# Optimization experiments

Measured on AMD Instinct MI355X. Metric: run time of the kernel, lower is better.

## Reference

```python
import jax, jax.numpy as jnp
import numpy as np

B, N, F_, H = 4, 2048, 1024, 16
DH = F_ // H
SCALE = F_ / 19.5  # module uses feats/19.5, not sqrt(head_dim)


def setup_inputs() -> dict:
    key = jax.random.key(0)
    ks = jax.random.split(key, 9)
    s = 1.0 / np.sqrt(F_)
    return {
        "x": jax.random.normal(ks[0], (B, N, F_), jnp.float32),
        "Wq": jax.random.normal(ks[1], (F_, F_), jnp.float32) * s,
        "bq": jax.random.normal(ks[2], (F_,), jnp.float32) * s,
        "Wk": jax.random.normal(ks[3], (F_, F_), jnp.float32) * s,
        "bk": jax.random.normal(ks[4], (F_,), jnp.float32) * s,
        "Wv": jax.random.normal(ks[5], (F_, F_), jnp.float32) * s,
        "bv": jax.random.normal(ks[6], (F_,), jnp.float32) * s,
        "Wo": jax.random.normal(ks[7], (F_, F_), jnp.float32) * s,
        "bo": jax.random.normal(ks[8], (F_,), jnp.float32) * s,
    }


def reference(x, Wq, bq, Wk, bk, Wv, bv, Wo, bo):
    b, n, f = x.shape
    # torch Linear: x @ W.T + b; then view(b,n,h,dh).transpose(1,2) -> bhnd
    def proj(W, bias):
        return (x @ W.T + bias).reshape(b, n, H, DH).transpose(0, 2, 1, 3)

    q = proj(Wq, bq)  # [b,h,n,dh]
    k = proj(Wk, bk)
    v = proj(Wv, bv)
    score = jax.nn.softmax(jnp.einsum("bhif,bhjf->bhij", q, k) / SCALE, axis=-1)
    attn = jnp.einsum("bhij,bhjf->bihf", score, v)  # [b,n,h,dh]
    o = attn.reshape(b, n, f) @ Wo.T + bo  # dropout p=0.0 -> identity
    return o
```

## Files before the change

kernel.cpp:

```cpp
#include <hip/hip_runtime.h>
#include <stdint.h>

typedef unsigned short u16;
typedef __bf16 bf16x8 __attribute__((ext_vector_type(8)));
typedef float f32x4 __attribute__((ext_vector_type(4)));

#define QSCALE (19.5f/1024.0f * 1.44269504088896340736f)

#define EXPB 16251.0f

__device__ __forceinline__ u16 f2bf(float f){
  uint32_t u = __float_as_uint(f);
  return (u16)((u + 0x7FFFu + ((u >> 16) & 1u)) >> 16);
}

__device__ __forceinline__ uint64_t cvt4(float4 f){
  union{ u16 u[4]; uint64_t v; } pk;
  pk.u[0]=f2bf(f.x); pk.u[1]=f2bf(f.y); pk.u[2]=f2bf(f.z); pk.u[3]=f2bf(f.w);
  return pk.v;
}

#define GLD_LDS16(g,l) __builtin_amdgcn_global_load_lds( \
    (const __attribute__((address_space(1))) void*)(g),  \
    (__attribute__((address_space(3))) void*)(l), 16, 0, 0)

__global__ __launch_bounds__(256) void k_prep(
    const float4* __restrict__ x,  const float4* __restrict__ Wq,
    const float4* __restrict__ Wk, const float4* __restrict__ Wv,
    const float4* __restrict__ Wo,
    const float4* __restrict__ bq, const float4* __restrict__ bk, const float4* __restrict__ bv,
    uint64_t* __restrict__ xb, uint64_t* __restrict__ wqkv, uint64_t* __restrict__ wob,
    float4* __restrict__ bqkv)
{
  const int NX = 2097152, NW = 262144;
  const int total = NX + 4*NW + 768;
  int i = blockIdx.x*256 + threadIdx.x;
  const int stride = gridDim.x*256;
  for (; i < total; i += stride){
    if (i < NX)             xb[i] = cvt4(x[i]);
    else if (i < NX+NW)     { int j = i-NX;      wqkv[j]      = cvt4(Wq[j]); }
    else if (i < NX+2*NW)   { int j = i-NX-NW;   wqkv[NW+j]   = cvt4(Wk[j]); }
    else if (i < NX+3*NW)   { int j = i-NX-2*NW; wqkv[2*NW+j] = cvt4(Wv[j]); }
    else if (i < NX+4*NW)   { int j = i-NX-3*NW; wob[j]       = cvt4(Wo[j]); }
    else {
      int j = i - NX - 4*NW;
      bqkv[j] = (j < 256) ? bq[j] : (j < 512 ? bk[j-256] : bv[j-512]);
    }
  }
}

template<int MODE>
__global__ __launch_bounds__(256) void gemm_bt(
    const u16* __restrict__ A, const u16* __restrict__ Bw,
    const float* __restrict__ bias, float* __restrict__ Cout,
    u16* __restrict__ q_ws, u16* __restrict__ k_ws, u16* __restrict__ v_ws)
{
  __shared__ u16 lds[3*8192];
  const int tid  = threadIdx.x;
  const int w    = tid >> 6, lane = tid & 63;
  const int wr   = w >> 1,  wc   = w & 1;
  const int g    = lane >> 4, c16 = lane & 15;
  const int nt   = blockIdx.x, mt = blockIdx.y;
  const size_t arow0 = (size_t)mt * 128, brow0 = (size_t)nt * 128;

  f32x4 acc[4][4] = {};

  const int srow  = w*16 + (lane >> 2);
  const int schk  = ((lane & 3) ^ ((lane >> 2) & 3)) * 8;
  const u16* gA = A  + (arow0 + srow)*1024 + schk;
  const u16* gB = Bw + (brow0 + srow)*1024 + schk;

  u16* ldsA0 = &lds[w*512];
  u16* ldsB0 = &lds[4096 + w*512];

  const int rswz = (g ^ (c16 & 3)) * 8;
  const int abase = (wr*64 + c16)*32 + rswz;
  const int bbase = 4096 + (wc*64 + c16)*32 + rswz;

#define GSTAGE(B2) do{ \
    GLD_LDS16(gA,          ldsA0 + (B2)*8192); \
    GLD_LDS16(gA + 65536,  ldsA0 + (B2)*8192 + 2048); \
    GLD_LDS16(gB,          ldsB0 + (B2)*8192); \
    GLD_LDS16(gB + 65536,  ldsB0 + (B2)*8192 + 2048); \
    gA += 32; gB += 32; \
  }while(0)

#define GBODY(B, STG, VMW) do{ \
    if (STG) GSTAGE(((B)+2)%3); \
    bf16x8 af[4], bfr[4]; \
    _Pragma("unroll") \
    for (int m = 0; m < 4; m++) \
      af[m]  = __builtin_bit_cast(bf16x8, *(const uint4*)(&lds[(B)*8192 + abase + m*512])); \
    _Pragma("unroll") \
    for (int n = 0; n < 4; n++) \
      bfr[n] = __builtin_bit_cast(bf16x8, *(const uint4*)(&lds[(B)*8192 + bbase + n*512])); \
    __builtin_amdgcn_s_setprio(1); \
    _Pragma("unroll") \
    for (int m = 0; m < 4; m++) \
      _Pragma("unroll") \
      for (int n = 0; n < 4; n++) \
        acc[m][n] = __builtin_amdgcn_mfma_f32_16x16x32_bf16(af[m], bfr[n], acc[m][n], 0, 0, 0); \
    __builtin_amdgcn_s_setprio(0); \
    if ((VMW) == 4){ asm volatile("s_waitcnt vmcnt(4)" ::: "memory"); __builtin_amdgcn_s_barrier(); } \
    else if ((VMW) == 0){ asm volatile("s_waitcnt vmcnt(0)" ::: "memory"); __builtin_amdgcn_s_barrier(); } \
  }while(0)

  GSTAGE(0); GSTAGE(1);
  asm volatile("s_waitcnt vmcnt(4)" ::: "memory");
  __builtin_amdgcn_s_barrier();

  #pragma unroll 1
  for (int rr = 0; rr < 10; rr++){
    GBODY(0, 1, 4);
    GBODY(1, 1, 4);
    GBODY(2, 1, 4);
  }
  GBODY(0, 0, 0);
  GBODY(1, 0, -1);

#undef GBODY
#undef GSTAGE

  #pragma unroll
  for (int m = 0; m < 4; m++){
    const size_t i0 = arow0 + wr*64 + m*16 + g*4;
    #pragma unroll
    for (int n = 0; n < 4; n++){
      const int o = (int)brow0 + wc*64 + n*16 + c16;
      const float bias_v = bias[o];
      if (MODE == 0){
        const int proj = o >> 10, wi = o & 1023, hh = wi >> 6, dd = wi & 63;
        if (proj < 2){
          u16* base = (proj == 0) ? q_ws : k_ws;
          const float sc = (proj == 0) ? QSCALE : 1.0f;
          #pragma unroll
          for (int r = 0; r < 4; r++){
            const size_t i = i0 + r;
            const size_t bb = i >> 11, nn = i & 2047;
            base[((bb*16 + hh)*2048 + nn)*64 + dd] = f2bf((acc[m][n][r] + bias_v)*sc);
          }
        } else {
          const size_t bb = i0 >> 11, nn = i0 & 2047;
          union{ u16 u[4]; uint64_t v; } pk;
          #pragma unroll
          for (int r = 0; r < 4; r++) pk.u[r] = f2bf(acc[m][n][r] + bias_v);
          *reinterpret_cast<uint64_t*>(v_ws + ((bb*16 + hh)*64 + dd)*2048 + nn) = pk.v;
        }
      } else {
        #pragma unroll
        for (int r = 0; r < 4; r++)
          Cout[(i0 + r)*1024 + o] = acc[m][n][r] + bias_v;
      }
    }
  }
}

__global__ __launch_bounds__(256, 2) void attn_k(
    const u16* __restrict__ Q, const u16* __restrict__ Kb, const u16* __restrict__ Vt,
    u16* __restrict__ O)
{
  __shared__ u16 lds[3*8192];
  const int tid = threadIdx.x, w = tid >> 6, lane = tid & 63;
  const int g = lane >> 4, l16 = lane & 15;

  const int f   = ((blockIdx.x & 7) << 6) | (blockIdx.x >> 3);
  const int qt_ = f & 7, bh = f >> 3;
  const int b = bh >> 4, h = bh & 15;
  const size_t hb = (size_t)bh * 2048 * 64;

  const int qrow0 = qt_*256 + w*64 + l16;
  bf16x8 qf[4][2];
  #pragma unroll
  for (int qt = 0; qt < 4; qt++)
    #pragma unroll
    for (int kc = 0; kc < 2; kc++)
      qf[qt][kc] = __builtin_bit_cast(bf16x8,
        *(const uint4*)(Q + hb + (size_t)(qrow0 + qt*16)*64 + kc*32 + g*8));

  f32x4 acc[4][4] = {};
  f32x4 lacc[4] = {};

  union{ u16 u[8]; bf16x8 f; } one_;
  #pragma unroll
  for (int i = 0; i < 8; i++) one_.u[i] = 0x3F80;
  const bf16x8 onesv = one_.f;

  const int srowL = w*8 + (lane >> 3);
  const int schunk = ((lane & 7) ^ ((lane >> 3) & 7)) * 8;
  const u16* gKs = Kb + hb + (size_t)srowL*64   + schunk;
  const u16* gVs = Vt + hb + (size_t)srowL*2048 + schunk;

  u16* ldsK0 = &lds[w*512];
  u16* ldsV0 = &lds[4096 + w*512];

  const int kb0 = l16*64 + (g ^ (l16 & 7))*8;
  const int kb1 = kb0 ^ 32;
  const int vswz = l16 & 7, vlo = (g & 1)*4, vg2 = g >> 1;
  int vb[2][2];
  #pragma unroll
  for (int p = 0; p < 2; p++)
    #pragma unroll
    for (int pc = 0; pc < 2; pc++)
      vb[p][pc] = l16*64 + (((p*4 + pc*2 + vg2) ^ vswz) << 3) + vlo;

#define STAGE_T(B2) do{ \
    GLD_LDS16(gKs,          ldsK0 + (B2)*8192); \
    GLD_LDS16(gKs + 2048,   ldsK0 + (B2)*8192 + 2048); \
    GLD_LDS16(gVs,          ldsV0 + (B2)*8192); \
    GLD_LDS16(gVs + 65536,  ldsV0 + (B2)*8192 + 2048); \
    gKs += 4096; gVs += 64; \
  }while(0)

#define BODY_T(B, STG, VMW) do{ \
    if (STG) STAGE_T(((B)+2)%3); \
    _Pragma("unroll") \
    for (int p = 0; p < 2; p++){ \
      uint64_t pkk[2][4]; \
      _Pragma("unroll") \
      for (int jh = 0; jh < 2; jh++){ \
        const int jt = p*2 + jh; \
        bf16x8 kf0 = __builtin_bit_cast(bf16x8, *(const uint4*)(&lds[(B)*8192 + jt*1024] + kb0)); \
        bf16x8 kf1 = __builtin_bit_cast(bf16x8, *(const uint4*)(&lds[(B)*8192 + jt*1024] + kb1)); \
        _Pragma("unroll") \
        for (int qt = 0; qt < 4; qt++){ \
          f32x4 st = {0.f,0.f,0.f,0.f}; \
          st = __builtin_amdgcn_mfma_f32_16x16x32_bf16(kf0, qf[qt][0], st, 0, 0, 0); \
          st = __builtin_amdgcn_mfma_f32_16x16x32_bf16(kf1, qf[qt][1], st, 0, 0, 0); \
          const uint32_t e0 = (uint32_t)(int)fmaf(st[0], 128.f, EXPB); \
          const uint32_t e1 = (uint32_t)(int)fmaf(st[1], 128.f, EXPB); \
          const uint32_t e2 = (uint32_t)(int)fmaf(st[2], 128.f, EXPB); \
          const uint32_t e3 = (uint32_t)(int)fmaf(st[3], 128.f, EXPB); \
          pkk[jh][qt] = (uint64_t)(e0 & 0xFFFFu) | ((uint64_t)(e1 & 0xFFFFu) << 16) \
                      | ((uint64_t)(e2 & 0xFFFFu) << 32) | ((uint64_t)e3 << 48); \
        } \
      } \
      union { uint64_t v[2]; bf16x8 f; } pf[4]; \
      _Pragma("unroll") \
      for (int qt = 0; qt < 4; qt++){ pf[qt].v[0] = pkk[0][qt]; pf[qt].v[1] = pkk[1][qt]; } \
      __builtin_amdgcn_s_setprio(1); \
      _Pragma("unroll") \
      for (int qt = 0; qt < 4; qt++) \
        lacc[qt] = __builtin_amdgcn_mfma_f32_16x16x32_bf16(onesv, pf[qt].f, lacc[qt], 0, 0, 0); \
      _Pragma("unroll") \
      for (int dt = 0; dt < 4; dt++){ \
        union { uint64_t v[2]; bf16x8 f; } vf; \
        vf.v[0] = *(const uint64_t*)(&lds[(B)*8192 + 4096 + dt*1024] + vb[p][0]); \
        vf.v[1] = *(const uint64_t*)(&lds[(B)*8192 + 4096 + dt*1024] + vb[p][1]); \
        _Pragma("unroll") \
        for (int qt = 0; qt < 4; qt++) \
          acc[dt][qt] = __builtin_amdgcn_mfma_f32_16x16x32_bf16(vf.f, pf[qt].f, acc[dt][qt], 0, 0, 0); \
      } \
      __builtin_amdgcn_s_setprio(0); \
    } \
    if ((VMW) == 4){ asm volatile("s_waitcnt vmcnt(4)" ::: "memory"); __builtin_amdgcn_s_barrier(); } \
    else if ((VMW) == 0){ asm volatile("s_waitcnt vmcnt(0)" ::: "memory"); __builtin_amdgcn_s_barrier(); } \
  }while(0)

  STAGE_T(0); STAGE_T(1);
  asm volatile("s_waitcnt vmcnt(4)" ::: "memory");
  __builtin_amdgcn_s_barrier();

  #pragma unroll 1
  for (int rr = 0; rr < 10; rr++){
    BODY_T(0, 1, 4);
    BODY_T(1, 1, 4);
    BODY_T(2, 1, 4);
  }
  BODY_T(0, 0, 0);
  BODY_T(1, 0, -1);

#undef BODY_T
#undef STAGE_T

  float inv[4];
  #pragma unroll
  for (int qt = 0; qt < 4; qt++) inv[qt] = 1.f / lacc[qt][0];

  #pragma unroll
  for (int qt = 0; qt < 4; qt++){
    const size_t ob = (((size_t)(b*2048 + qrow0 + qt*16))*16 + h)*64;
    #pragma unroll
    for (int dt = 0; dt < 4; dt++){
      union{ u16 u[4]; uint64_t v; } pkk;
      #pragma unroll
      for (int r = 0; r < 4; r++) pkk.u[r] = f2bf(acc[dt][qt][r] * inv[qt]);
      *reinterpret_cast<uint64_t*>(O + ob + dt*16 + g*4) = pkk.v;
    }
  }
}

extern "C" void kernel_launch(void* const* d_in, const int* in_sizes, int n_in,
                              void* d_out, int out_size, void* d_ws, size_t ws_size,
                              hipStream_t stream)
{
  const float* x  = (const float*)d_in[0];
  const float* Wq = (const float*)d_in[1];
  const float* bq = (const float*)d_in[2];
  const float* Wk = (const float*)d_in[3];
  const float* bk = (const float*)d_in[4];
  const float* Wv = (const float*)d_in[5];
  const float* bv = (const float*)d_in[6];
  const float* Wo = (const float*)d_in[7];
  const float* bo = (const float*)d_in[8];
  float* out = (float*)d_out;

  char* ws = (char*)d_ws;
  size_t off = 0;
  auto bump = [&](size_t bytes){ size_t o = off; off = (off + bytes + 255) & ~(size_t)255; return o; };
  u16*  xb   = (u16*)  (ws + bump(8388608ull*2));
  u16*  wqkv = (u16*)  (ws + bump(3145728ull*2));
  u16*  wob  = (u16*)  (ws + bump(1048576ull*2));
  float* bqkv= (float*)(ws + bump(3072ull*4));
  u16*  qws  = (u16*)  (ws + bump(8388608ull*2));
  u16*  kws  = (u16*)  (ws + bump(8388608ull*2));
  u16*  vws  = (u16*)  (ws + bump(8388608ull*2));
  u16*  att  = (u16*)  (ws + bump(8388608ull*2));

  k_prep<<<2048, 256, 0, stream>>>(
      (const float4*)x, (const float4*)Wq, (const float4*)Wk, (const float4*)Wv, (const float4*)Wo,
      (const float4*)bq, (const float4*)bk, (const float4*)bv,
      (uint64_t*)xb, (uint64_t*)wqkv, (uint64_t*)wob, (float4*)bqkv);

  gemm_bt<0><<<dim3(24, 64), 256, 0, stream>>>(xb, wqkv, bqkv, nullptr, qws, kws, vws);
  attn_k<<<512, 256, 0, stream>>>(qws, kws, vws, att);
  gemm_bt<1><<<dim3(8, 64), 256, 0, stream>>>(att, wob, bo, out, nullptr, nullptr, nullptr);
}
```

Measured before the change: 169.7 us.

## Use 256x256-tile 8-wave GEMM for QKV projection and retune LDS swizzle

Replaces the 128x128 QKV projection GEMM with a dedicated 256x256 tile kernel using 512 threads. It double-buffers K=64 slices in 128KB of LDS, interleaves global-to-LDS staging with MFMA phases, and raises wave priority around the MFMAs. The larger tile roughly halves global/LDS traffic per flop. The trade-off is one block per CU, fewer blocks (384), and tighter barrier-driven pipelining. The output-projection GEMM also gets a different LDS XOR swizzle to reduce bank conflicts.

```diff
diff --git a/kernel.cpp b/kernel.cpp
--- a/kernel.cpp
+++ b/kernel.cpp
@@ -6,7 +6,6 @@
 typedef float f32x4 __attribute__((ext_vector_type(4)));
 
 #define QSCALE (19.5f/1024.0f * 1.44269504088896340736f)
-
 #define EXPB 16251.0f
 
 __device__ __forceinline__ u16 f2bf(float f){
@@ -49,11 +48,122 @@
   }
 }
 
-template<int MODE>
-__global__ __launch_bounds__(256) void gemm_bt(
+__global__ __launch_bounds__(512, 1) void gemm256(
     const u16* __restrict__ A, const u16* __restrict__ Bw,
-    const float* __restrict__ bias, float* __restrict__ Cout,
+    const float* __restrict__ bias,
     u16* __restrict__ q_ws, u16* __restrict__ k_ws, u16* __restrict__ v_ws)
+{
+  __shared__ u16 lds[65536];
+  const int tid = threadIdx.x;
+  const int w = tid >> 6, lane = tid & 63;
+  const int wr = w >> 2, wc = w & 3;
+  const int g = lane >> 4, c16 = lane & 15;
+  const int nt = blockIdx.x, mt = blockIdx.y;
+  const size_t arow0 = (size_t)mt * 256, brow0 = (size_t)nt * 256;
+
+  f32x4 acc[8][4] = {};
+
+  const int schunk8 = ((tid & 7) ^ ((tid >> 3) & 7)) * 8;
+  const u16* gA = A  + (arow0 + (tid >> 3)) * 1024 + schunk8;
+  const u16* gB = Bw + (brow0 + (tid >> 3)) * 1024 + schunk8;
+  const int wdst = w * 512;
+
+  const int ks0 = (g ^ (c16 & 7)) * 8;
+  const int ard = (wr*64 + c16) * 64;
+  const int brd = 16384 + (wc*32 + c16) * 64;
+
+#define G2STAGE(SMAT, SHALF, SBUF, KOFF) do{ \
+    const u16* s_ = (SMAT) ? gB : gA; \
+    GLD_LDS16(s_ + ((SHALF)*128 + 0)*1024 + (KOFF), \
+              &lds[(SBUF)*32768 + (SMAT)*16384 + (SHALF)*8192 + wdst]); \
+    GLD_LDS16(s_ + ((SHALF)*128 + 64)*1024 + (KOFF), \
+              &lds[(SBUF)*32768 + (SMAT)*16384 + (SHALF)*8192 + 4096 + wdst]); \
+  }while(0)
+
+#define PHASE8(MH, NH, RB, DOSTG, SMAT, SHALF, SBUF, SKOFF, VMW) do{ \
+    bf16x8 af[4][2], bfv[2][2]; \
+    _Pragma("unroll") \
+    for (int mi = 0; mi < 4; mi++){ \
+      af[mi][0] = __builtin_bit_cast(bf16x8, *(const uint4*)(&lds[(RB)*32768 + (MH)*8192 + ard + mi*1024 + ks0])); \
+      af[mi][1] = __builtin_bit_cast(bf16x8, *(const uint4*)(&lds[(RB)*32768 + (MH)*8192 + ard + mi*1024 + (ks0^32)])); \
+    } \
+    _Pragma("unroll") \
+    for (int ni = 0; ni < 2; ni++){ \
+      bfv[ni][0] = __builtin_bit_cast(bf16x8, *(const uint4*)(&lds[(RB)*32768 + brd + (NH)*8192 + ni*1024 + ks0])); \
+      bfv[ni][1] = __builtin_bit_cast(bf16x8, *(const uint4*)(&lds[(RB)*32768 + brd + (NH)*8192 + ni*1024 + (ks0^32)])); \
+    } \
+    if (DOSTG) G2STAGE(SMAT, SHALF, SBUF, SKOFF); \
+    __builtin_amdgcn_s_barrier(); \
+    asm volatile("s_waitcnt lgkmcnt(0)" ::: "memory"); \
+    __builtin_amdgcn_sched_barrier(0); \
+    __builtin_amdgcn_s_setprio(1); \
+    _Pragma("unroll") \
+    for (int mi = 0; mi < 4; mi++) \
+      _Pragma("unroll") \
+      for (int ni = 0; ni < 2; ni++){ \
+        acc[(MH)*4+mi][(NH)*2+ni] = __builtin_amdgcn_mfma_f32_16x16x32_bf16(af[mi][0], bfv[ni][0], acc[(MH)*4+mi][(NH)*2+ni], 0, 0, 0); \
+        acc[(MH)*4+mi][(NH)*2+ni] = __builtin_amdgcn_mfma_f32_16x16x32_bf16(af[mi][1], bfv[ni][1], acc[(MH)*4+mi][(NH)*2+ni], 0, 0, 0); \
+      } \
+    __builtin_amdgcn_s_setprio(0); \
+    if ((VMW) == 4)      asm volatile("s_waitcnt vmcnt(4)" ::: "memory"); \
+    else if ((VMW) == 0) asm volatile("s_waitcnt vmcnt(0)" ::: "memory"); \
+    __builtin_amdgcn_s_barrier(); \
+  }while(0)
+
+  G2STAGE(0,0,0,0); G2STAGE(0,1,0,0); G2STAGE(1,0,0,0); G2STAGE(1,1,0,0);
+  G2STAGE(0,0,1,64); G2STAGE(0,1,1,64); G2STAGE(1,0,1,64); G2STAGE(1,1,1,64);
+  asm volatile("s_waitcnt vmcnt(8)" ::: "memory");
+  __builtin_amdgcn_s_barrier();
+
+  #pragma unroll 1
+  for (int i = 0; i < 8; i++){
+    const int kb = i*128;
+    const int s01 = (i > 0), s27 = (i < 7);
+    const int vm3 = s27 ? 4 : 0, vm7 = s27 ? 4 : -1;
+    PHASE8(0,0, 0, s01, 0,1,1, kb+64,  -1);
+    PHASE8(0,1, 0, s01, 1,1,1, kb+64,  -1);
+    PHASE8(1,0, 0, s27, 0,0,0, kb+128, -1);
+    PHASE8(1,1, 0, s27, 1,0,0, kb+128, vm3);
+    PHASE8(0,0, 1, s27, 0,1,0, kb+128, -1);
+    PHASE8(0,1, 1, s27, 1,1,0, kb+128, -1);
+    PHASE8(1,0, 1, s27, 0,0,1, kb+192, -1);
+    PHASE8(1,1, 1, s27, 1,0,1, kb+192, vm7);
+  }
+
+#undef PHASE8
+#undef G2STAGE
+
+  #pragma unroll
+  for (int m = 0; m < 8; m++){
+    const size_t i0 = arow0 + (size_t)((m>>2)*128 + wr*64 + (m&3)*16 + g*4);
+    #pragma unroll
+    for (int n = 0; n < 4; n++){
+      const int o = (int)brow0 + (n>>1)*128 + wc*32 + (n&1)*16 + c16;
+      const float bias_v = bias[o];
+      const int proj = o >> 10, wi = o & 1023, hh = wi >> 6, dd = wi & 63;
+      if (proj < 2){
+        u16* base = (proj == 0) ? q_ws : k_ws;
+        const float sc = (proj == 0) ? QSCALE : 1.0f;
+        #pragma unroll
+        for (int r = 0; r < 4; r++){
+          const size_t i = i0 + r;
+          const size_t bb = i >> 11, nn = i & 2047;
+          base[((bb*16 + hh)*2048 + nn)*64 + dd] = f2bf((acc[m][n][r] + bias_v)*sc);
+        }
+      } else {
+        const size_t bb = i0 >> 11, nn = i0 & 2047;
+        union{ u16 u[4]; uint64_t v; } pk;
+        #pragma unroll
+        for (int r = 0; r < 4; r++) pk.u[r] = f2bf(acc[m][n][r] + bias_v);
+        *reinterpret_cast<uint64_t*>(v_ws + ((bb*16 + hh)*64 + dd)*2048 + nn) = pk.v;
+      }
+    }
+  }
+}
+
+__global__ __launch_bounds__(256) void gemm_bt1(
+    const u16* __restrict__ A, const u16* __restrict__ Bw,
+    const float* __restrict__ bias, float* __restrict__ Cout)
 {
   __shared__ u16 lds[3*8192];
   const int tid  = threadIdx.x;
@@ -66,14 +176,14 @@
   f32x4 acc[4][4] = {};
 
   const int srow  = w*16 + (lane >> 2);
-  const int schk  = ((lane & 3) ^ ((lane >> 2) & 3)) * 8;
+  const int schk  = ((lane & 3) ^ ((lane >> 3) & 3)) * 8;
   const u16* gA = A  + (arow0 + srow)*1024 + schk;
   const u16* gB = Bw + (brow0 + srow)*1024 + schk;
 
   u16* ldsA0 = &lds[w*512];
   u16* ldsB0 = &lds[4096 + w*512];
 
-  const int rswz = (g ^ (c16 & 3)) * 8;
+  const int rswz = (g ^ ((c16 >> 1) & 3)) * 8;
   const int abase = (wr*64 + c16)*32 + rswz;
   const int bbase = 4096 + (wc*64 + c16)*32 + rswz;
 
@@ -128,29 +238,9 @@
     for (int n = 0; n < 4; n++){
       const int o = (int)brow0 + wc*64 + n*16 + c16;
       const float bias_v = bias[o];
-      if (MODE == 0){
-        const int proj = o >> 10, wi = o & 1023, hh = wi >> 6, dd = wi & 63;
-        if (proj < 2){
-          u16* base = (proj == 0) ? q_ws : k_ws;
-          const float sc = (proj == 0) ? QSCALE : 1.0f;
-          #pragma unroll
-          for (int r = 0; r < 4; r++){
-            const size_t i = i0 + r;
-            const size_t bb = i >> 11, nn = i & 2047;
-            base[((bb*16 + hh)*2048 + nn)*64 + dd] = f2bf((acc[m][n][r] + bias_v)*sc);
-          }
-        } else {
-          const size_t bb = i0 >> 11, nn = i0 & 2047;
-          union{ u16 u[4]; uint64_t v; } pk;
-          #pragma unroll
-          for (int r = 0; r < 4; r++) pk.u[r] = f2bf(acc[m][n][r] + bias_v);
-          *reinterpret_cast<uint64_t*>(v_ws + ((bb*16 + hh)*64 + dd)*2048 + nn) = pk.v;
-        }
-      } else {
-        #pragma unroll
-        for (int r = 0; r < 4; r++)
-          Cout[(i0 + r)*1024 + o] = acc[m][n][r] + bias_v;
-      }
+      #pragma unroll
+      for (int r = 0; r < 4; r++)
+        Cout[(i0 + r)*1024 + o] = acc[m][n][r] + bias_v;
     }
   }
 }
@@ -321,7 +411,7 @@
       (const float4*)bq, (const float4*)bk, (const float4*)bv,
       (uint64_t*)xb, (uint64_t*)wqkv, (uint64_t*)wob, (float4*)bqkv);
 
-  gemm_bt<0><<<dim3(24, 64), 256, 0, stream>>>(xb, wqkv, bqkv, nullptr, qws, kws, vws);
+  gemm256<<<dim3(12, 32), 512, 0, stream>>>(xb, wqkv, bqkv, qws, kws, vws);
   attn_k<<<512, 256, 0, stream>>>(qws, kws, vws, att);
-  gemm_bt<1><<<dim3(8, 64), 256, 0, stream>>>(att, wob, bo, out, nullptr, nullptr, nullptr);
-}
+  gemm_bt1<<<dim3(8, 64), 256, 0, stream>>>(att, wob, bo, out);
+}
```

Result: slower. 179.0 us (+5.5%).
